# Optimization experiments

Hardware: AMD Instinct MI355X
Metric: run time of the kernel (lower is better)

## Reference

```python
import jax, jax.numpy as jnp
import numpy as np

SCALE = 4


def _dist_mats():
    # Replicates matrix_generation() with scale=4 (numpy constants).
    s = SCALE
    x = np.array([-2.0, -1.0, 1.0, 2.0], np.float32)  # arange(-2,3) with the 0 removed
    base = np.broadcast_to(x[None, :], (s, s)).copy()  # varies along width
    dm = np.stack([base, base.T])[None]                # [1,2,4,4]
    xr = np.broadcast_to(np.arange(1, s + 1, dtype=np.float32)[None, :], (s, s)).copy()
    xc = xr.T
    dm1 = dm.copy(); dm1[:, 0] = s - xr + 1
    dm2 = dm.copy(); dm2[:, 0] = xr
    dm3 = dm.copy(); dm3[:, 1] = s - xc + 1
    dm4 = dm.copy(); dm4[:, 1] = xc
    # NOTE: forward() reuses dm1..dm4 for the 4 diagonal directions (as in the
    # original code, which indexes self.distance_matrix1..4 for matrices 5..8).
    return dm, dm1, dm2, dm3, dm4


def _mlp(x, w0, w1, w2, w3):
    # 1x1-conv stack 66->32->16->8->1, no bias, LeakyReLU(0.01) between.
    h = jax.nn.leaky_relu(jnp.einsum('bchw,oc->bohw', x, w0))
    h = jax.nn.leaky_relu(jnp.einsum('bchw,oc->bohw', h, w1))
    h = jax.nn.leaky_relu(jnp.einsum('bchw,oc->bohw', h, w2))
    return jnp.einsum('bchw,oc->bohw', h, w3)


def setup_inputs() -> dict:
    key = jax.random.key(0)
    ks = jax.random.split(key, 8)
    B, C, H, W = 2, 32, 256, 512
    lr_feature = jax.random.normal(ks[0], (B, C, H // SCALE, W // SCALE), jnp.float32)
    hr_feature = jax.random.normal(ks[1], (B, C, H, W), jnp.float32)
    lr_feature_r = jax.random.normal(ks[2], (B, C, H // SCALE, W // SCALE), jnp.float32)
    hr_feature_r = jax.random.normal(ks[3], (B, C, H, W), jnp.float32)
    # kaiming_normal_(mode='fan_out') for 1x1 conv: std = sqrt(2 / out_ch)
    def kaiming(k, shape):
        return jax.random.normal(k, shape, jnp.float32) * np.sqrt(2.0 / shape[0]).astype(np.float32)
    w0 = kaiming(ks[4], (32, 66))
    w1 = kaiming(ks[5], (16, 32))
    w2 = kaiming(ks[6], (8, 16))
    w3 = kaiming(ks[7], (1, 8))
    return {'lr_feature': lr_feature, 'hr_feature': hr_feature,
            'lr_feature_r': lr_feature_r, 'hr_feature_r': hr_feature_r,
            'w0': w0, 'w1': w1, 'w2': w2, 'w3': w3}


def reference(lr_feature, hr_feature, lr_feature_r, hr_feature_r, w0, w1, w2, w3):
    s = SCALE
    B, _, H, W = hr_feature.shape
    dm, dm1, dm2, dm3, dm4 = _dist_mats()
    tile = lambda d: jnp.tile(jnp.asarray(d), (B, 1, H // s, W // s))  # [B,2,H,W]
    D, D1, D2, D3, D4 = tile(dm), tile(dm1), tile(dm2), tile(dm3), tile(dm4)
    # nearest-neighbor upsample of lr feature by scale in both spatial dims
    lr = jnp.repeat(jnp.repeat(lr_feature, s, axis=3), s, axis=2)
    hr = hr_feature
    pad1 = jnp.full((B, 1, H, s), -100.0, hr.dtype)  # width padding
    pad2 = jnp.full((B, 1, s, W), -100.0, hr.dtype)  # height padding
    cat = lambda *xs: jnp.concatenate(xs, axis=1)
    m = lambda x: _mlp(x, w0, w1, w2, w3)

    w_c = m(cat(lr, hr, D))
    w_l = jnp.concatenate([pad1, m(cat(lr[:, :, :, :-s], hr[:, :, :, s:], D1[:, :, :, :-s]))], -1)
    w_r = jnp.concatenate([m(cat(lr[:, :, :, s:], hr[:, :, :, :-s], D2[:, :, :, s:])), pad1], -1)
    w_t = jnp.concatenate([pad2, m(cat(lr[:, :, :-s, :], hr[:, :, s:, :], D3[:, :, :-s, :]))], -2)
    w_b = jnp.concatenate([m(cat(lr[:, :, s:, :], hr[:, :, :-s, :], D4[:, :, s:, :])), pad2], -2)
    w_lt = jnp.concatenate([pad2, jnp.concatenate(
        [pad1[:, :, s:, :], m(cat(lr[:, :, :-s, :-s], hr[:, :, s:, s:], D1[:, :, :-s, :-s]))], -1)], -2)
    w_rt = jnp.concatenate([pad2, jnp.concatenate(
        [m(cat(lr[:, :, :-s, s:], hr[:, :, s:, :-s], D2[:, :, :-s, s:])), pad1[:, :, s:, :]], -1)], -2)
    w_lb = jnp.concatenate([jnp.concatenate(
        [pad1[:, :, s:, :], m(cat(lr[:, :, s:, :-s], hr[:, :, :-s, s:], D3[:, :, s:, :-s]))], -1), pad2], -2)
    w_rb = jnp.concatenate([jnp.concatenate(
        [m(cat(lr[:, :, s:, s:], hr[:, :, :-s, :-s], D4[:, :, s:, s:])), pad1[:, :, :-s, :]], -1), pad2], -2)

    weight_all = jnp.concatenate([w_c, w_l, w_r, w_t, w_b, w_lt, w_rt, w_lb, w_rb], axis=1)
    # Original returns the 9 channel slices of softmax(weight_all, dim=1);
    # we return the full normalized [B,9,H,W] tensor (slice i == output i).
    return jax.nn.softmax(weight_all, axis=1)
```

## Files before the change

kernel.cpp:

```cpp
#include <hip/hip_runtime.h>
#include <math.h>

#define SC 4
#define BB 2
#define CC 32
#define HH 256
#define WW 512
#define CH (HH / SC)
#define CW (WW / SC)

using f16x8 = __attribute__((ext_vector_type(8))) _Float16;
using f32x4 = __attribute__((ext_vector_type(4))) float;

__device__ __constant__ int c_dh[9] = {0, 0, 0, -1, 1, -1, -1, 1, 1};
__device__ __constant__ int c_dw[9] = {0, -1, 1, 0, 0, -1, 1, -1, 1};
__device__ __constant__ int c_s0[9] = {0, 1, 2, 0, 0, 1, 2, 0, 0};
__device__ __constant__ int c_s1[9] = {0, 0, 0, 1, 2, 0, 0, 1, 2};

__global__ __launch_bounds__(256) void alr_prepass(const float* __restrict__ lr,
                                                   const float* __restrict__ w0,
                                                   float* __restrict__ alr) {
    const int idx = blockIdx.x * 256 + threadIdx.x;
    if (idx >= BB * CH * CW) return;
    const int b = idx / (CH * CW);
    const int cell = idx - b * (CH * CW);
    const float* lp = lr + (size_t)b * CC * CH * CW + cell;
    float lv[32];
#pragma unroll
    for (int c = 0; c < 32; c++) lv[c] = lp[(size_t)c * (CH * CW)];
    float acc[32];
#pragma unroll
    for (int o = 0; o < 32; o++) {
        float a = 0.f;
#pragma unroll
        for (int c = 0; c < 32; c++) a = fmaf(lv[c], w0[o * 66 + c], a);
        acc[o] = a;
    }
    float4* op = (float4*)(alr + (size_t)idx * 32);
#pragma unroll
    for (int j = 0; j < 8; j++)
        op[j] = make_float4(acc[4 * j], acc[4 * j + 1], acc[4 * j + 2], acc[4 * j + 3]);
}

template <bool USE_WS>
__global__ __launch_bounds__(256, 4) void ercm_mfma(const float* __restrict__ hr,
                                                    const float* __restrict__ lr,
                                                    const float* __restrict__ alr,
                                                    const float* __restrict__ w0,
                                                    const float* __restrict__ w1,
                                                    const float* __restrict__ w2,
                                                    const float* __restrict__ w3,
                                                    float* __restrict__ out) {
    __shared__ _Float16 s_alr[54 * 40];
    __shared__ _Float16 s_ahr[4][64 * 40];
    __shared__ _Float16 s_d2[4][16 * 24];
    __shared__ float    s_part[4][64 * 12];
    __shared__ float    s_lg[9][256];

    const int tid = threadIdx.x;
    const int lane = tid & 63;
    const int ty = tid >> 6;
    const int m16 = lane & 15;
    const int q = lane >> 4;
    const int bx = blockIdx.x;
    const int by = blockIdx.y;
    const int b = blockIdx.z;
    const int h = by * 4 + ty;
    const int wp0 = bx * 64;
    const size_t HW = (size_t)HH * WW;

    const int cy0 = by, cx0 = bx * 16;
    if (USE_WS) {
        for (int i = tid; i < 54 * 32; i += 256) {
            const int c = i & 31, cell = i >> 5;
            const int row = cell / 18, col = cell - row * 18;
            const int gcy = cy0 - 1 + row, gcx = cx0 - 1 + col;
            float v = 0.f;
            if ((unsigned)gcy < (unsigned)CH && (unsigned)gcx < (unsigned)CW)
                v = alr[(((size_t)b * CH + gcy) * CW + gcx) * 32 + c];
            s_alr[cell * 40 + c] = (_Float16)v;
        }
    } else {
        for (int i = tid; i < 54 * 32; i += 256) {
            const int o = i & 31, cell = i >> 5;
            const int row = cell / 18, col = cell - row * 18;
            const int gcy = cy0 - 1 + row, gcx = cx0 - 1 + col;
            float a = 0.f;
            if ((unsigned)gcy < (unsigned)CH && (unsigned)gcx < (unsigned)CW) {
                const float* lp = lr + (size_t)b * CC * CH * CW + (size_t)gcy * CW + gcx;
#pragma unroll
                for (int c = 0; c < 32; c++) a = fmaf(lp[(size_t)c * (CH * CW)], w0[o * 66 + c], a);
            }
            s_alr[cell * 40 + o] = (_Float16)a;
        }
    }

    f16x8 w1B, w0hB0, w0hB1, w2B;
    {
        const float* p1 = w1 + m16 * 32 + q * 8;
        const float* p00 = w0 + m16 * 66 + 32 + q * 8;
        const float* p01 = w0 + (m16 + 16) * 66 + 32 + q * 8;
        const bool w2ok = (m16 < 8) && (q < 2);
#pragma unroll
        for (int j = 0; j < 8; j++) {
            w1B[j] = (_Float16)p1[j];
            w0hB0[j] = (_Float16)p00[j];
            w0hB1[j] = (_Float16)p01[j];
            w2B[j] = (_Float16)(w2ok ? w2[m16 * 16 + q * 8 + j] : 0.f);
        }
    }
    float w0d0[8], w0d1[8];
#pragma unroll
    for (int j = 0; j < 8; j++) {
        w0d0[j] = w0[(q * 8 + j) * 66 + 64];
        w0d1[j] = w0[(q * 8 + j) * 66 + 65];
    }
    const float w3v = (m16 < 8) ? w3[m16] : 0.f;

    const float* hp = hr + (size_t)b * CC * HW + (size_t)h * WW + wp0;
#pragma unroll 1
    for (int t = 0; t < 4; t++) {
        const int px = t * 16 + m16;
        f16x8 a;
#pragma unroll
        for (int j = 0; j < 8; j++) a[j] = (_Float16)hp[(size_t)(q * 8 + j) * HW + px];
        f32x4 acc0 = {0.f, 0.f, 0.f, 0.f}, acc1 = {0.f, 0.f, 0.f, 0.f};
        acc0 = __builtin_amdgcn_mfma_f32_16x16x32_f16(a, w0hB0, acc0, 0, 0, 0);
        acc1 = __builtin_amdgcn_mfma_f32_16x16x32_f16(a, w0hB1, acc1, 0, 0, 0);
#pragma unroll
        for (int r = 0; r < 4; r++) {
            const int pxr = t * 16 + q * 4 + r;
            s_ahr[ty][pxr * 40 + m16] = (_Float16)acc0[r];
            s_ahr[ty][pxr * 40 + 16 + m16] = (_Float16)acc1[r];
        }
    }

    const int xm = m16 & 3;
    const float xv = (float)(xm < 2 ? xm - 2 : xm - 1);
    const float x1 = (float)(4 - xm), x2 = (float)(xm + 1);
    const int ym = h & 3;
    const float yv = (float)(ym < 2 ? ym - 2 : ym - 1);
    const float y1 = (float)(4 - ym), y2 = (float)(ym + 1);

    __syncthreads();

#pragma unroll 1
    for (int d = 0; d < 9; d++) {
        const int dh = c_dh[d], dw = c_dw[d];
        const int sel0 = c_s0[d], sel1 = c_s1[d];
        const float d0 = (sel0 == 0) ? xv : ((sel0 == 1) ? x1 : x2);
        const float d1 = (sel1 == 0) ? yv : ((sel1 == 1) ? y1 : y2);

#pragma unroll 1
        for (int t = 0; t < 4; t++) {
            const int pxm = t * 16 + m16;
            const int cell = (1 + dh) * 18 + (1 + dw + (pxm >> 2));
            const f16x8 ah = *(const f16x8*)&s_ahr[ty][pxm * 40 + q * 8];
            const f16x8 al = *(const f16x8*)&s_alr[cell * 40 + q * 8];
            f16x8 a1;
#pragma unroll
            for (int j = 0; j < 8; j++) {
                float v = (float)ah[j] + (float)al[j];
                v = fmaf(d0, w0d0[j], v);
                v = fmaf(d1, w0d1[j], v);
                v = fmaxf(v, 0.01f * v);
                a1[j] = (_Float16)v;
            }
            f32x4 acc2 = {0.f, 0.f, 0.f, 0.f};
            acc2 = __builtin_amdgcn_mfma_f32_16x16x32_f16(a1, w1B, acc2, 0, 0, 0);
#pragma unroll
            for (int r = 0; r < 4; r++) {
                float v = acc2[r];
                v = fmaxf(v, 0.01f * v);
                s_d2[ty][(q * 4 + r) * 24 + m16] = (_Float16)v;
            }
            f16x8 a3;
#pragma unroll
            for (int j = 0; j < 8; j++) a3[j] = (_Float16)0.f;
            if (q < 2) a3 = *(const f16x8*)&s_d2[ty][m16 * 24 + q * 8];
            f32x4 acc3 = {0.f, 0.f, 0.f, 0.f};
            acc3 = __builtin_amdgcn_mfma_f32_16x16x32_f16(a3, w2B, acc3, 0, 0, 0);
            if (m16 < 8) {
#pragma unroll
                for (int r = 0; r < 4; r++) {
                    float v = acc3[r];
                    v = fmaxf(v, 0.01f * v);
                    s_part[ty][(t * 16 + q * 4 + r) * 12 + m16] = w3v * v;
                }
            }
        }
        const float4 p0 = *(const float4*)&s_part[ty][lane * 12];
        const float4 p1 = *(const float4*)&s_part[ty][lane * 12 + 4];
        const float lg = ((p0.x + p0.y) + (p0.z + p0.w)) + ((p1.x + p1.y) + (p1.z + p1.w));
        const int wpix = wp0 + lane;
        const bool valid = ((unsigned)(h + 4 * dh) < (unsigned)HH) &&
                           ((unsigned)(wpix + 4 * dw) < (unsigned)WW);
        s_lg[d][tid] = valid ? lg : -100.0f;
    }

    float l[9];
#pragma unroll
    for (int d = 0; d < 9; d++) l[d] = s_lg[d][tid];
    float m = l[0];
#pragma unroll
    for (int d = 1; d < 9; d++) m = fmaxf(m, l[d]);
    float s = 0.f;
#pragma unroll
    for (int d = 0; d < 9; d++) {
        l[d] = __expf(l[d] - m);
        s += l[d];
    }
    const float inv = __builtin_amdgcn_rcpf(s);
    float* op = out + (size_t)b * 9 * HW + (size_t)h * WW + wp0 + lane;
#pragma unroll
    for (int d = 0; d < 9; d++) op[(size_t)d * HW] = l[d] * inv;
}

extern "C" void kernel_launch(void* const* d_in, const int* in_sizes, int n_in,
                              void* d_out, int out_size, void* d_ws, size_t ws_size,
                              hipStream_t stream) {
    const float* lr = (const float*)d_in[0];
    const float* hr = (const float*)d_in[1];
    const float* w0 = (const float*)d_in[4];
    const float* w1 = (const float*)d_in[5];
    const float* w2 = (const float*)d_in[6];
    const float* w3 = (const float*)d_in[7];
    float* out = (float*)d_out;

    const size_t alr_bytes = (size_t)BB * CH * CW * 32 * sizeof(float);
    dim3 grid(WW / 64, HH / 4, BB);

    if (ws_size >= alr_bytes) {
        float* alr = (float*)d_ws;
        alr_prepass<<<(BB * CH * CW + 255) / 256, 256, 0, stream>>>(lr, w0, alr);
        ercm_mfma<true><<<grid, 256, 0, stream>>>(hr, lr, alr, w0, w1, w2, w3, out);
    } else {
        ercm_mfma<false><<<grid, 256, 0, stream>>>(hr, lr, nullptr, w0, w1, w2, w3, out);
    }
}
```

Before: 162.7 us.

## Restructure per-tile loop: fuse direction loop, DPP reductions, packed math, in-register softmax

Reorders the loops so each 16-pixel tile computes its hr projection and then all nine directions with the direction loop fully unrolled. The final 8-wide w3 dot product is reduced across lanes with DPP adds instead of round-tripping through shared memory, and the softmax runs per tile in registers. Layer-1 elementwise math uses packed f32x2 operations. This shrinks shared memory and drops the s_part/s_lg staging, at the cost of only 4 of 16 lanes writing outputs, which gives narrower, less coalesced stores.

```diff
diff --git a/kernel.cpp b/kernel.cpp
--- a/kernel.cpp
+++ b/kernel.cpp
@@ -11,11 +11,28 @@
 
 using f16x8 = __attribute__((ext_vector_type(8))) _Float16;
 using f32x4 = __attribute__((ext_vector_type(4))) float;
-
-__device__ __constant__ int c_dh[9] = {0, 0, 0, -1, 1, -1, -1, 1, 1};
-__device__ __constant__ int c_dw[9] = {0, -1, 1, 0, 0, -1, 1, -1, 1};
-__device__ __constant__ int c_s0[9] = {0, 1, 2, 0, 0, 1, 2, 0, 0};
-__device__ __constant__ int c_s1[9] = {0, 0, 0, 1, 2, 0, 0, 1, 2};
+using f32x2 = __attribute__((ext_vector_type(2))) float;
+
+constexpr int K_dh[9] = {0, 0, 0, -1, 1, -1, -1, 1, 1};
+constexpr int K_dw[9] = {0, -1, 1, 0, 0, -1, 1, -1, 1};
+constexpr int K_s0[9] = {0, 1, 2, 0, 0, 1, 2, 0, 0};
+constexpr int K_s1[9] = {0, 0, 0, 1, 2, 0, 0, 1, 2};
+
+template <int CTRL>
+__device__ __forceinline__ float dpp_add(float v) {
+    union { float f; int i; } u, r;
+    u.f = v;
+    r.i = __builtin_amdgcn_update_dpp(0, u.i, CTRL, 0xF, 0xF, true);
+    return v + r.f;
+}
+
+__device__ __forceinline__ float sum16(float v) {
+    v = dpp_add<0xB1>(v);
+    v = dpp_add<0x4E>(v);
+    v = dpp_add<0x141>(v);
+    v = dpp_add<0x140>(v);
+    return v;
+}
 
 __global__ __launch_bounds__(256) void alr_prepass(const float* __restrict__ lr,
                                                    const float* __restrict__ w0,
@@ -52,10 +69,8 @@
                                                     const float* __restrict__ w3,
                                                     float* __restrict__ out) {
     __shared__ _Float16 s_alr[54 * 40];
-    __shared__ _Float16 s_ahr[4][64 * 40];
-    __shared__ _Float16 s_d2[4][16 * 24];
-    __shared__ float    s_part[4][64 * 12];
-    __shared__ float    s_lg[9][256];
+    __shared__ _Float16 s_ahr[4][16 * 40];
+    __shared__ _Float16 s_d2[4][16 * 40];
 
     const int tid = threadIdx.x;
     const int lane = tid & 63;
@@ -109,31 +124,13 @@
             w2B[j] = (_Float16)(w2ok ? w2[m16 * 16 + q * 8 + j] : 0.f);
         }
     }
-    float w0d0[8], w0d1[8];
-#pragma unroll
-    for (int j = 0; j < 8; j++) {
-        w0d0[j] = w0[(q * 8 + j) * 66 + 64];
-        w0d1[j] = w0[(q * 8 + j) * 66 + 65];
+    f32x2 w0d0v[4], w0d1v[4];
+#pragma unroll
+    for (int jp = 0; jp < 4; jp++) {
+        w0d0v[jp] = f32x2{w0[(q * 8 + 2 * jp) * 66 + 64], w0[(q * 8 + 2 * jp + 1) * 66 + 64]};
+        w0d1v[jp] = f32x2{w0[(q * 8 + 2 * jp) * 66 + 65], w0[(q * 8 + 2 * jp + 1) * 66 + 65]};
     }
     const float w3v = (m16 < 8) ? w3[m16] : 0.f;
-
-    const float* hp = hr + (size_t)b * CC * HW + (size_t)h * WW + wp0;
-#pragma unroll 1
-    for (int t = 0; t < 4; t++) {
-        const int px = t * 16 + m16;
-        f16x8 a;
-#pragma unroll
-        for (int j = 0; j < 8; j++) a[j] = (_Float16)hp[(size_t)(q * 8 + j) * HW + px];
-        f32x4 acc0 = {0.f, 0.f, 0.f, 0.f}, acc1 = {0.f, 0.f, 0.f, 0.f};
-        acc0 = __builtin_amdgcn_mfma_f32_16x16x32_f16(a, w0hB0, acc0, 0, 0, 0);
-        acc1 = __builtin_amdgcn_mfma_f32_16x16x32_f16(a, w0hB1, acc1, 0, 0, 0);
-#pragma unroll
-        for (int r = 0; r < 4; r++) {
-            const int pxr = t * 16 + q * 4 + r;
-            s_ahr[ty][pxr * 40 + m16] = (_Float16)acc0[r];
-            s_ahr[ty][pxr * 40 + 16 + m16] = (_Float16)acc1[r];
-        }
-    }
 
     const int xm = m16 & 3;
     const float xv = (float)(xm < 2 ? xm - 2 : xm - 1);
@@ -142,78 +139,96 @@
     const float yv = (float)(ym < 2 ? ym - 2 : ym - 1);
     const float y1 = (float)(4 - ym), y2 = (float)(ym + 1);
 
+    _Float16* sa = s_ahr[ty];
+    _Float16* sd = s_d2[ty];
+#pragma unroll
+    for (int r = 0; r < 4; r++) sd[(q * 4 + r) * 40 + 16 + m16] = (_Float16)0.f;
+
     __syncthreads();
 
+    const float* hp = hr + (size_t)b * CC * HW + (size_t)h * WW + wp0;
+
 #pragma unroll 1
-    for (int d = 0; d < 9; d++) {
-        const int dh = c_dh[d], dw = c_dw[d];
-        const int sel0 = c_s0[d], sel1 = c_s1[d];
-        const float d0 = (sel0 == 0) ? xv : ((sel0 == 1) ? x1 : x2);
-        const float d1 = (sel1 == 0) ? yv : ((sel1 == 1) ? y1 : y2);
-
-#pragma unroll 1
-        for (int t = 0; t < 4; t++) {
-            const int pxm = t * 16 + m16;
-            const int cell = (1 + dh) * 18 + (1 + dw + (pxm >> 2));
-            const f16x8 ah = *(const f16x8*)&s_ahr[ty][pxm * 40 + q * 8];
-            const f16x8 al = *(const f16x8*)&s_alr[cell * 40 + q * 8];
+    for (int t = 0; t < 4; t++) {
+        f16x8 a;
+#pragma unroll
+        for (int j = 0; j < 8; j++) a[j] = (_Float16)hp[(size_t)(q * 8 + j) * HW + t * 16 + m16];
+        f32x4 acc0 = {0.f, 0.f, 0.f, 0.f}, acc1 = {0.f, 0.f, 0.f, 0.f};
+        acc0 = __builtin_amdgcn_mfma_f32_16x16x32_f16(a, w0hB0, acc0, 0, 0, 0);
+        acc1 = __builtin_amdgcn_mfma_f32_16x16x32_f16(a, w0hB1, acc1, 0, 0, 0);
+#pragma unroll
+        for (int r = 0; r < 4; r++) {
+            sa[(q * 4 + r) * 40 + m16] = (_Float16)acc0[r];
+            sa[(q * 4 + r) * 40 + 16 + m16] = (_Float16)acc1[r];
+        }
+        const f16x8 ahv = *(const f16x8*)&sa[m16 * 40 + q * 8];
+        f32x2 ah2[4];
+#pragma unroll
+        for (int jp = 0; jp < 4; jp++)
+            ah2[jp] = f32x2{(float)ahv[2 * jp], (float)ahv[2 * jp + 1]};
+
+        const _Float16* alp = &s_alr[((t * 16 + m16) >> 2) * 40 + q * 8];
+        const int wown = wp0 + t * 16 + q * 4 + xm;
+
+        float l[9];
+#pragma unroll
+        for (int d = 0; d < 9; d++) {
+            const int dh = K_dh[d], dw = K_dw[d];
+            const float d0 = (K_s0[d] == 0) ? xv : ((K_s0[d] == 1) ? x1 : x2);
+            const float d1 = (K_s1[d] == 0) ? yv : ((K_s1[d] == 1) ? y1 : y2);
+            const f32x2 d0v = {d0, d0}, d1v = {d1, d1};
+
+            const f16x8 alv = *(const f16x8*)(alp + ((1 + dh) * 18 + (1 + dw)) * 40);
             f16x8 a1;
 #pragma unroll
-            for (int j = 0; j < 8; j++) {
-                float v = (float)ah[j] + (float)al[j];
-                v = fmaf(d0, w0d0[j], v);
-                v = fmaf(d1, w0d1[j], v);
-                v = fmaxf(v, 0.01f * v);
-                a1[j] = (_Float16)v;
+            for (int jp = 0; jp < 4; jp++) {
+                f32x2 v = ah2[jp] + f32x2{(float)alv[2 * jp], (float)alv[2 * jp + 1]};
+                v = __builtin_elementwise_fma(w0d0v[jp], d0v, v);
+                v = __builtin_elementwise_fma(w0d1v[jp], d1v, v);
+                v = __builtin_elementwise_max(v, v * 0.01f);
+                a1[2 * jp] = (_Float16)v[0];
+                a1[2 * jp + 1] = (_Float16)v[1];
             }
             f32x4 acc2 = {0.f, 0.f, 0.f, 0.f};
             acc2 = __builtin_amdgcn_mfma_f32_16x16x32_f16(a1, w1B, acc2, 0, 0, 0);
 #pragma unroll
             for (int r = 0; r < 4; r++) {
-                float v = acc2[r];
-                v = fmaxf(v, 0.01f * v);
-                s_d2[ty][(q * 4 + r) * 24 + m16] = (_Float16)v;
+                const float v = fmaxf(acc2[r], 0.01f * acc2[r]);
+                sd[(q * 4 + r) * 40 + m16] = (_Float16)v;
             }
-            f16x8 a3;
-#pragma unroll
-            for (int j = 0; j < 8; j++) a3[j] = (_Float16)0.f;
-            if (q < 2) a3 = *(const f16x8*)&s_d2[ty][m16 * 24 + q * 8];
+            const f16x8 a3 = *(const f16x8*)&sd[m16 * 40 + q * 8];
             f32x4 acc3 = {0.f, 0.f, 0.f, 0.f};
             acc3 = __builtin_amdgcn_mfma_f32_16x16x32_f16(a3, w2B, acc3, 0, 0, 0);
-            if (m16 < 8) {
-#pragma unroll
-                for (int r = 0; r < 4; r++) {
-                    float v = acc3[r];
-                    v = fmaxf(v, 0.01f * v);
-                    s_part[ty][(t * 16 + q * 4 + r) * 12 + m16] = w3v * v;
-                }
-            }
-        }
-        const float4 p0 = *(const float4*)&s_part[ty][lane * 12];
-        const float4 p1 = *(const float4*)&s_part[ty][lane * 12 + 4];
-        const float lg = ((p0.x + p0.y) + (p0.z + p0.w)) + ((p1.x + p1.y) + (p1.z + p1.w));
-        const int wpix = wp0 + lane;
-        const bool valid = ((unsigned)(h + 4 * dh) < (unsigned)HH) &&
-                           ((unsigned)(wpix + 4 * dw) < (unsigned)WW);
-        s_lg[d][tid] = valid ? lg : -100.0f;
-    }
-
-    float l[9];
-#pragma unroll
-    for (int d = 0; d < 9; d++) l[d] = s_lg[d][tid];
-    float m = l[0];
-#pragma unroll
-    for (int d = 1; d < 9; d++) m = fmaxf(m, l[d]);
-    float s = 0.f;
-#pragma unroll
-    for (int d = 0; d < 9; d++) {
-        l[d] = __expf(l[d] - m);
-        s += l[d];
-    }
-    const float inv = __builtin_amdgcn_rcpf(s);
-    float* op = out + (size_t)b * 9 * HW + (size_t)h * WW + wp0 + lane;
-#pragma unroll
-    for (int d = 0; d < 9; d++) op[(size_t)d * HW] = l[d] * inv;
+
+            float sr[4];
+#pragma unroll
+            for (int r = 0; r < 4; r++)
+                sr[r] = sum16(w3v * fmaxf(acc3[r], 0.01f * acc3[r]));
+            float lv = sr[0];
+            lv = (xm == 1) ? sr[1] : lv;
+            lv = (xm == 2) ? sr[2] : lv;
+            lv = (xm == 3) ? sr[3] : lv;
+            const bool ok = ((unsigned)(h + 4 * dh) < (unsigned)HH) &&
+                            ((unsigned)(wown + 4 * dw) < (unsigned)WW);
+            l[d] = ok ? lv : -100.0f;
+        }
+
+        float mx = l[0];
+#pragma unroll
+        for (int d = 1; d < 9; d++) mx = fmaxf(mx, l[d]);
+        float s = 0.f;
+#pragma unroll
+        for (int d = 0; d < 9; d++) {
+            l[d] = __expf(l[d] - mx);
+            s += l[d];
+        }
+        const float inv = __builtin_amdgcn_rcpf(s);
+        if (m16 < 4) {
+            float* op = out + (size_t)b * 9 * HW + (size_t)h * WW + (wp0 + t * 16 + q * 4 + m16);
+#pragma unroll
+            for (int d = 0; d < 9; d++) op[(size_t)d * HW] = l[d] * inv;
+        }
+    }
 }
 
 extern "C" void kernel_launch(void* const* d_in, const int* in_sizes, int n_in,
```

After: 153.9 us. 1.06x faster.
